# Optimization experiments

Measured on AMD Instinct MI355X. Metric: run time of the kernel, lower is better.

Reference implementation:

```python
import jax, jax.numpy as jnp
import numpy as np

B, N, C = 2, 2048, 1024
H = 16
HD = C // H  # 64


def setup_inputs() -> dict:
    key = jax.random.key(0)
    ks = jax.random.split(key, 6)
    x = jax.random.normal(ks[0], (B, N, C), dtype=jnp.float32)
    # realistic rotary angles
    inv_freq = 1.0 / (10000.0 ** (np.arange(0, HD, 2, dtype=np.float32) / HD))
    t = np.arange(N, dtype=np.float32)
    freqs = np.outer(t, inv_freq)                      # [N, HD/2]
    emb = np.concatenate([freqs, freqs], axis=-1)      # [N, HD]
    cos = jnp.asarray(np.cos(emb), dtype=jnp.float32)
    sin = jnp.asarray(np.sin(emb), dtype=jnp.float32)
    qkv_w = jax.random.normal(ks[1], (3 * C, C), dtype=jnp.float32) * (1.0 / np.sqrt(C))
    proj_w = jax.random.normal(ks[2], (C, C), dtype=jnp.float32) * (1.0 / np.sqrt(C))
    proj_b = jnp.zeros((C,), dtype=jnp.float32)
    return {"x": x, "cos": cos, "sin": sin, "qkv_w": qkv_w, "proj_w": proj_w, "proj_b": proj_b}


def _apply_rope(x, cos, sin):
    # x: [B, H, N, HD]; cos/sin: [N, HD] (broadcast over B, H)
    x1, x2 = jnp.split(x, 2, axis=-1)
    rotated = jnp.concatenate([-x2, x1], axis=-1)
    return x * cos + rotated * sin


def reference(x, cos, sin, qkv_w, proj_w, proj_b):
    b, n, c = x.shape
    scale = (c // H) ** (-0.5)
    qkv = jnp.einsum('bnc,dc->bnd', x, qkv_w)          # [B, N, 3C]
    qkv = qkv.reshape(b, n, 3, H, HD).transpose(2, 0, 3, 1, 4)  # [3, B, H, N, HD]
    q, k, v = qkv[0], qkv[1], qkv[2]
    q = _apply_rope(q, cos, sin)
    k = _apply_rope(k, cos, sin)
    attn = jnp.einsum('bhid,bhjd->bhij', q, k) * scale  # [B, H, N, N]
    attn = jax.nn.softmax(attn, axis=-1)
    out = jnp.einsum('bhij,bhjd->bhid', attn, v)        # [B, H, N, HD]
    out = out.transpose(0, 2, 1, 3).reshape(b, n, c)    # [B, N, C]
    return jnp.einsum('bnc,dc->bnd', out, proj_w) + proj_b
```

## Files before the change

### kernel.cpp

```cpp
#include <hip/hip_runtime.h>
#include <stdint.h>

typedef __bf16 bf16;
typedef bf16 bf16x8 __attribute__((ext_vector_type(8)));
typedef float f32x4 __attribute__((ext_vector_type(4)));
typedef float f32x16 __attribute__((ext_vector_type(16)));
typedef unsigned short u16x8 __attribute__((ext_vector_type(8)));
typedef unsigned short u16x4 __attribute__((ext_vector_type(4)));

__device__ __forceinline__ unsigned short f2bfu(float f) {
    union { bf16 h; unsigned short u; } x;
    x.h = (bf16)f;
    return x.u;
}
__device__ __forceinline__ float bfu2f(unsigned short u) {
    union { unsigned int i; float f; } x;
    x.i = ((unsigned int)u) << 16;
    return x.f;
}
__device__ __forceinline__ unsigned int pack2bf(float a, float b) {
    union { bf16 h[2]; unsigned int u; } x;
    x.h[0] = (bf16)a; x.h[1] = (bf16)b;
    return x.u;
}
__device__ __forceinline__ void pl32_swap(unsigned int &a, unsigned int &b) {
    asm volatile("v_permlane32_swap_b32 %0, %1" : "+v"(a), "+v"(b));
}

__device__ __forceinline__ void gld_lds16(const void* g, void* l) {
    __builtin_amdgcn_global_load_lds(
        (const __attribute__((address_space(1))) unsigned int*)(uintptr_t)g,
        (__attribute__((address_space(3))) unsigned int*)(unsigned int)(uintptr_t)l,
        16, 0, 0);
}

__global__ void cast_bf16_kernel(const float* __restrict__ in,
                                 unsigned short* __restrict__ out, int n8) {
    int i = blockIdx.x * blockDim.x + threadIdx.x;
    if (i >= n8) return;
    const f32x4* p = (const f32x4*)(in + (size_t)i * 8);
    f32x4 a = p[0], b = p[1];
    u16x8 o;
    o[0]=f2bfu(a[0]); o[1]=f2bfu(a[1]); o[2]=f2bfu(a[2]); o[3]=f2bfu(a[3]);
    o[4]=f2bfu(b[0]); o[5]=f2bfu(b[1]); o[6]=f2bfu(b[2]); o[7]=f2bfu(b[3]);
    *(u16x8*)(out + (size_t)i * 8) = o;
}

__global__ void rope_kernel(unsigned short* __restrict__ qkv,
                            const float* __restrict__ cosp,
                            const float* __restrict__ sinp) {
    int tid = blockIdx.x * blockDim.x + threadIdx.x;
    int i8  = tid & 3;
    int h   = (tid >> 2) & 15;
    int sel = (tid >> 6) & 1;
    int n   = (tid >> 7) & 2047;
    int b   = tid >> 18;
    size_t base = ((size_t)(b*2048 + n))*3072 + sel*1024 + h*64 + i8*8;
    u16x8 x1 = *(u16x8*)(qkv + base);
    u16x8 x2 = *(u16x8*)(qkv + base + 32);
    const f32x4* cp = (const f32x4*)(cosp + n*64 + i8*8);
    const f32x4* sp = (const f32x4*)(sinp + n*64 + i8*8);
    f32x4 c0 = cp[0], c1 = cp[1], s0 = sp[0], s1 = sp[1];
    float scale = sel ? 1.0f : (0.125f * 1.44269504088896f);
    u16x8 o1, o2;
#pragma unroll
    for (int j = 0; j < 8; j++) {
        float cc = (j < 4) ? c0[j] : c1[j-4];
        float ss = (j < 4) ? s0[j] : s1[j-4];
        float a = bfu2f(x1[j]), d = bfu2f(x2[j]);
        o1[j] = f2bfu((a*cc - d*ss) * scale);
        o2[j] = f2bfu((d*cc + a*ss) * scale);
    }
    *(u16x8*)(qkv + base)      = o1;
    *(u16x8*)(qkv + base + 32) = o2;
}

__global__ __launch_bounds__(512, 2) void gemm_qkv8(
    const unsigned short* __restrict__ A, const unsigned short* __restrict__ B,
    unsigned short* __restrict__ C, int M, int N, int K)
{
    extern __shared__ char smem[];
    int nwgx = gridDim.x;
    int nwg  = nwgx * gridDim.y;
    int orig = blockIdx.y * nwgx + blockIdx.x;
    int cpx  = nwg >> 3;
    int wg   = (orig & 7) * cpx + (orig >> 3);
    int bx = wg % nwgx, by = wg / nwgx;
    int m0 = by << 8, n0 = bx << 8;
    int t  = threadIdx.x;
    int wv = t >> 6, l = t & 63;
    int fr = l & 15, fq = l >> 4;
    int wm = (wv >> 2) << 7;
    int wn = (wv & 3) << 6;
    int aswz = (fr & 3) << 4;

    auto stage = [&](int kt, int bsel) {
        int k0 = kt << 5;
        char* base = smem + (bsel << 15);
#pragma unroll
        for (int j = 0; j < 2; ++j) {
            int y   = (j << 13) + t * 16;
            int ly  = y ^ (((y >> 6) & 3) << 4);
            int row = ly >> 6;
            int colu = (ly & 63) >> 1;
            gld_lds16(A + (size_t)(m0 + row) * K + k0 + colu,
                      base + ((j << 13) + (wv << 10)));
            gld_lds16(B + (size_t)(n0 + row) * K + k0 + colu,
                      base + 16384 + ((j << 13) + (wv << 10)));
        }
    };

    f32x4 acc[8][4];
#pragma unroll
    for (int m = 0; m < 8; ++m)
#pragma unroll
        for (int n = 0; n < 4; ++n) acc[m][n] = f32x4{0.f, 0.f, 0.f, 0.f};

    stage(0, 0);
    stage(1, 1);
    int cb = 0;
    for (int kt = 0; kt < 32; ++kt) {
        if (kt < 31) asm volatile("s_waitcnt vmcnt(4)" ::: "memory");
        else         asm volatile("s_waitcnt vmcnt(0)" ::: "memory");
        __builtin_amdgcn_s_barrier();
        if (kt + 2 < 32) {
            int sb = cb - 1; if (sb < 0) sb = 2;
            stage(kt + 2, sb);
        }
        const char* base = smem + (cb << 15);
        const char* Ab = base + ((wm + fr) << 6) + ((fq * 16) ^ aswz);
        const char* Bb = base + 16384 + ((wn + fr) << 6) + ((fq * 16) ^ aswz);
        bf16x8 bfr[4], af[4];
#pragma unroll
        for (int n = 0; n < 4; ++n) bfr[n] = *(const bf16x8*)(Bb + (n << 10));
#pragma unroll
        for (int m = 0; m < 4; ++m) af[m]  = *(const bf16x8*)(Ab + (m << 10));
        __builtin_amdgcn_s_barrier();
        __builtin_amdgcn_s_setprio(1);
#pragma unroll
        for (int m = 0; m < 4; ++m)
#pragma unroll
            for (int n = 0; n < 4; ++n)
                acc[m][n] = __builtin_amdgcn_mfma_f32_16x16x32_bf16(af[m], bfr[n], acc[m][n], 0, 0, 0);
        __builtin_amdgcn_s_setprio(0);
#pragma unroll
        for (int m = 0; m < 4; ++m) af[m] = *(const bf16x8*)(Ab + ((m + 4) << 10));
        __builtin_amdgcn_s_barrier();
        __builtin_amdgcn_s_setprio(1);
#pragma unroll
        for (int m = 0; m < 4; ++m)
#pragma unroll
            for (int n = 0; n < 4; ++n)
                acc[m + 4][n] = __builtin_amdgcn_mfma_f32_16x16x32_bf16(af[m], bfr[n], acc[m + 4][n], 0, 0, 0);
        __builtin_amdgcn_s_setprio(0);
        cb = (cb == 2) ? 0 : cb + 1;
    }
#pragma unroll
    for (int m = 0; m < 8; ++m)
#pragma unroll
        for (int n = 0; n < 4; ++n)
#pragma unroll
            for (int e = 0; e < 4; ++e) {
                int row = m0 + wm + m * 16 + fq * 4 + e;
                int col = n0 + wn + n * 16 + fr;
                C[(size_t)row * N + col] = f2bfu(acc[m][n][e]);
            }
}

template<int OUT_F32>
__global__ __launch_bounds__(256, 2) void gemm_bt(
    const unsigned short* __restrict__ A, const unsigned short* __restrict__ B,
    void* __restrict__ Cp, const float* __restrict__ bias,
    int M, int N, int K)
{
    __shared__ __align__(16) unsigned short As[2][128*32];
    __shared__ __align__(16) unsigned short Bs[2][128*32];
    int nwg  = gridDim.x * gridDim.y;
    int orig = blockIdx.y * gridDim.x + blockIdx.x;
    int qq = nwg >> 3, rr = nwg & 7;
    int xcd = orig & 7, idx = orig >> 3;
    int wg = (xcd < rr) ? (xcd*(qq+1) + idx) : (rr*(qq+1) + (xcd-rr)*qq + idx);
    int bx = wg % gridDim.x, by = wg / gridDim.x;
    int m0 = by * 128, n0 = bx * 128;
    int t = threadIdx.x;
    int w = t >> 6, l = t & 63;
    int c = l & 15, g = l >> 4;
    int wm = (w >> 1) * 64, wn = (w & 1) * 64;

    auto stage = [&](int kt, int bsel) {
#pragma unroll
        for (int r2 = 0; r2 < 2; ++r2) {
            int xb = w*2048 + r2*1024;
            int x  = xb + l*16;
            int row  = x >> 6;
            int colu = (x & 63) >> 1;
            int k0 = kt << 5;
            gld_lds16(A + (size_t)(m0+row)*K + k0 + colu, (void*)(As[bsel] + (xb >> 1)));
            gld_lds16(B + (size_t)(n0+row)*K + k0 + colu, (void*)(Bs[bsel] + (xb >> 1)));
        }
    };

    f32x4 acc[4][4];
#pragma unroll
    for (int i = 0; i < 4; i++)
#pragma unroll
        for (int j = 0; j < 4; j++) acc[i][j] = f32x4{0.f,0.f,0.f,0.f};

    int nkt = K >> 5;
    stage(0, 0);
    int cur = 0;
    for (int kt = 0; kt < nkt; ++kt) {
        __syncthreads();
        if (kt + 1 < nkt) stage(kt + 1, cur ^ 1);
        const unsigned short* Ab = As[cur] + wm*32;
        const unsigned short* Bb = Bs[cur] + wn*32;
        bf16x8 af[4], bfr[4];
#pragma unroll
        for (int i = 0; i < 4; i++) af[i]  = *(const bf16x8*)(Ab + (i*16+c)*32 + g*8);
#pragma unroll
        for (int i = 0; i < 4; i++) bfr[i] = *(const bf16x8*)(Bb + (i*16+c)*32 + g*8);
#pragma unroll
        for (int i = 0; i < 4; i++)
#pragma unroll
            for (int j = 0; j < 4; j++)
                acc[i][j] = __builtin_amdgcn_mfma_f32_16x16x32_bf16(af[i], bfr[j], acc[i][j], 0, 0, 0);
        cur ^= 1;
    }
#pragma unroll
    for (int i = 0; i < 4; i++)
#pragma unroll
        for (int j = 0; j < 4; j++)
#pragma unroll
            for (int e = 0; e < 4; e++) {
                int row = m0 + wm + i*16 + g*4 + e;
                int col = n0 + wn + j*16 + c;
                float v = acc[i][j][e];
                if (bias) v += bias[col];
                if (OUT_F32) ((float*)Cp)[(size_t)row*N + col] = v;
                else ((unsigned short*)Cp)[(size_t)row*N + col] = f2bfu(v);
            }
}

__global__ __launch_bounds__(256, 2) void attn_kernel(
    const unsigned short* __restrict__ qkv, unsigned short* __restrict__ outp)
{
    __shared__ __align__(16) unsigned short Ks[2][64*64];
    __shared__ __align__(16) unsigned short Vt[2][64*64];
    int bh = blockIdx.y;
    int b = bh >> 4, h = bh & 15;
    int q0 = blockIdx.x << 7;
    int t = threadIdx.x;
    int w = t >> 6, l = t & 63;
    int q = l & 31, hi = l >> 5;
    int qw = q0 + w*32;
    size_t bh_base = ((size_t)b*2048)*3072 + (size_t)h*64;

    auto stageK = [&](int kv0, int bsel) {
#pragma unroll
        for (int r2 = 0; r2 < 2; ++r2) {
            int xb = w*2048 + r2*1024;
            int x  = xb + l*16;
            int row  = x >> 7;
            int scolb = (x & 127) ^ ((row & 7) << 4);
            gld_lds16(qkv + bh_base + 1024 + (size_t)(kv0 + row)*3072 + (scolb >> 1),
                      (void*)(Ks[bsel] + (xb >> 1)));
        }
    };
    auto loadV = [&](int kv0, u16x8 &v0, u16x8 &v1) {
        int p  = t >> 3;
        int hb = (t & 7) << 3;
        const unsigned short* src = qkv + bh_base + 2048 + (size_t)(kv0 + 2*p)*3072 + hb;
        v0 = *(const u16x8*)src;
        v1 = *(const u16x8*)(src + 3072);
    };
    auto writeV = [&](const u16x8 &v0, const u16x8 &v1, int bsel) {
        int p  = t >> 3;
        int hb = (t & 7) << 3;
#pragma unroll
        for (int e = 0; e < 8; e++) {
            int hd = hb + e;
            int colb = (4*p) ^ ((((hd) ^ (hd >> 3)) & 7) << 4);
            *(unsigned int*)((char*)Vt[bsel] + hd*128 + colb) =
                (unsigned int)v0[e] | ((unsigned int)v1[e] << 16);
        }
    };

    bf16x8 qf[4];
#pragma unroll
    for (int dc = 0; dc < 4; dc++)
        qf[dc] = *(const bf16x8*)(qkv + bh_base + (size_t)(qw + q)*3072 + dc*16 + hi*8);

    f32x16 oacc[2];
#pragma unroll
    for (int e = 0; e < 16; e++) { oacc[0][e] = 0.f; oacc[1][e] = 0.f; }
    float lsum = 0.f;

    u16x8 vc0, vc1, vn0, vn1;
    stageK(0, 0);
    loadV(0, vc0, vc1);
    int cur = 0;

    for (int kvt = 0; kvt < 32; ++kvt) {
        writeV(vc0, vc1, cur);
        __syncthreads();
        if (kvt < 31) {
            int kv0n = (kvt + 1) << 6;
            stageK(kv0n, cur ^ 1);
            loadV(kv0n, vn0, vn1);
        }
        const char* ksb = (const char*)Ks[cur];
        const char* vtb = (const char*)Vt[cur];

#pragma unroll
        for (int sblk = 0; sblk < 2; ++sblk) {
            f32x16 st;
#pragma unroll
            for (int e = 0; e < 16; e++) st[e] = 0.f;
            int krow = sblk*32 + q;
            int ksw = (krow & 7) << 4;
#pragma unroll
            for (int dc = 0; dc < 4; ++dc) {
                bf16x8 kf = *(const bf16x8*)(ksb + krow*128 + ((dc*32 + hi*16) ^ ksw));
                st = __builtin_amdgcn_mfma_f32_32x32x16_bf16(kf, qf[dc], st, 0, 0, 0);
            }
            unsigned int wds[8];
#pragma unroll
            for (int m = 0; m < 8; m++) {
                float p0 = __builtin_amdgcn_exp2f(st[2*m]);
                float p1 = __builtin_amdgcn_exp2f(st[2*m+1]);
                lsum += p0 + p1;
                wds[m] = pack2bf(p0, p1);
            }
#pragma unroll
            for (int half = 0; half < 2; ++half) {
                unsigned int a0 = wds[half*4 + 0], b0 = wds[half*4 + 2];
                unsigned int a1 = wds[half*4 + 1], b1 = wds[half*4 + 3];
                pl32_swap(a0, b0);
                pl32_swap(a1, b1);
                union { unsigned int u[4]; bf16x8 v; } pf;
                pf.u[0] = a0; pf.u[1] = a1; pf.u[2] = b0; pf.u[3] = b1;
                int kc = sblk*2 + half;
#pragma unroll
                for (int hdblk = 0; hdblk < 2; ++hdblk) {
                    int hd = hdblk*32 + q;
                    int vsw = ((hd ^ (hd >> 3)) & 7) << 4;
                    bf16x8 vf = *(const bf16x8*)(vtb + hd*128 + ((kc*32 + hi*16) ^ vsw));
                    oacc[hdblk] = __builtin_amdgcn_mfma_f32_32x32x16_bf16(vf, pf.v, oacc[hdblk], 0, 0, 0);
                }
            }
        }
        vc0 = vn0; vc1 = vn1;
        cur ^= 1;
    }
    float ltot = lsum + __shfl_xor(lsum, 32, 64);
    float rinv = 1.0f / ltot;
    size_t orow = (size_t)(b*2048 + qw + q) * 1024 + h*64;
#pragma unroll
    for (int hdblk = 0; hdblk < 2; ++hdblk)
#pragma unroll
        for (int quad = 0; quad < 4; ++quad) {
            u16x4 o4;
#pragma unroll
            for (int j = 0; j < 4; j++)
                o4[j] = f2bfu(oacc[hdblk][quad*4 + j] * rinv);
            *(u16x4*)(outp + orow + hdblk*32 + quad*8 + hi*4) = o4;
        }
}

extern "C" void kernel_launch(void* const* d_in, const int* in_sizes, int n_in,
                              void* d_out, int out_size, void* d_ws, size_t ws_size,
                              hipStream_t stream) {
    const float* x      = (const float*)d_in[0];
    const float* cosp   = (const float*)d_in[1];
    const float* sinp   = (const float*)d_in[2];
    const float* qkv_w  = (const float*)d_in[3];
    const float* proj_w = (const float*)d_in[4];
    const float* proj_b = (const float*)d_in[5];

    char* ws = (char*)d_ws;
    unsigned short* xb     = (unsigned short*)(ws);
    unsigned short* wqkvb  = (unsigned short*)(ws + (size_t)(8u << 20));
    unsigned short* wprojb = (unsigned short*)(ws + (size_t)(14u << 20));
    unsigned short* qkvb   = (unsigned short*)(ws + (size_t)(16u << 20));
    unsigned short* attno  = xb;

    cast_bf16_kernel<<<2048, 256, 0, stream>>>(x, xb, 524288);
    cast_bf16_kernel<<<1536, 256, 0, stream>>>(qkv_w, wqkvb, 393216);
    cast_bf16_kernel<<<512, 256, 0, stream>>>(proj_w, wprojb, 131072);

    hipFuncSetAttribute((const void*)gemm_qkv8,
                        hipFuncAttributeMaxDynamicSharedMemorySize, 98304);
    gemm_qkv8<<<dim3(12, 16), 512, 98304, stream>>>(xb, wqkvb, qkvb, 4096, 3072, 1024);
    rope_kernel<<<2048, 256, 0, stream>>>(qkvb, cosp, sinp);
    attn_kernel<<<dim3(16, 32), 256, 0, stream>>>(qkvb, attno);
    gemm_bt<1><<<dim3(8, 32), 256, 0, stream>>>(attno, wprojb, d_out, proj_b, 4096, 1024, 1024);
}
```

Measured before the change: 135.2 us.

## Split KV range across two wave groups per attention block and merge via LDS

The attention block grows from 4 to 8 waves. Each group of 4 waves handles half of the KV tiles for the same 128 queries, with its own double-buffered K/V staging in a 64KB LDS array. Because the softmax uses no running max, the two partial outputs and row sums are merged by a plain add through LDS before normalisation and the store. This halves the serial KV loop per block and raises resident waves, at the cost of an extra LDS reduction and tighter register limits from launch_bounds(512,4), which may cause spills.

```diff
diff --git a/kernel.cpp b/kernel.cpp
--- a/kernel.cpp
+++ b/kernel.cpp
@@ -241,46 +241,51 @@
             }
 }
 
-__global__ __launch_bounds__(256, 2) void attn_kernel(
+__global__ __launch_bounds__(512, 4) void attn_kernel(
     const unsigned short* __restrict__ qkv, unsigned short* __restrict__ outp)
 {
-    __shared__ __align__(16) unsigned short Ks[2][64*64];
-    __shared__ __align__(16) unsigned short Vt[2][64*64];
+    __shared__ __align__(16) char lds[65536];
     int bh = blockIdx.y;
     int b = bh >> 4, h = bh & 15;
     int q0 = blockIdx.x << 7;
     int t = threadIdx.x;
     int w = t >> 6, l = t & 63;
+    int pair = w >> 2, wp = w & 3;
+    int tp = t & 255;
     int q = l & 31, hi = l >> 5;
-    int qw = q0 + w*32;
+    int qw = q0 + wp*32;
     size_t bh_base = ((size_t)b*2048)*3072 + (size_t)h*64;
 
+    auto kbase = [&](int bsel) -> char* { return lds + (((pair << 1) | bsel) << 13); };
+    auto vbase = [&](int bsel) -> char* { return lds + 32768 + (((pair << 1) | bsel) << 13); };
+
     auto stageK = [&](int kv0, int bsel) {
 #pragma unroll
         for (int r2 = 0; r2 < 2; ++r2) {
-            int xb = w*2048 + r2*1024;
+            int xb = wp*2048 + r2*1024;
             int x  = xb + l*16;
             int row  = x >> 7;
             int scolb = (x & 127) ^ ((row & 7) << 4);
             gld_lds16(qkv + bh_base + 1024 + (size_t)(kv0 + row)*3072 + (scolb >> 1),
-                      (void*)(Ks[bsel] + (xb >> 1)));
+                      kbase(bsel) + xb);
         }
     };
     auto loadV = [&](int kv0, u16x8 &v0, u16x8 &v1) {
-        int p  = t >> 3;
-        int hb = (t & 7) << 3;
+        int p  = tp >> 3;
+        int hb = (tp & 7) << 3;
         const unsigned short* src = qkv + bh_base + 2048 + (size_t)(kv0 + 2*p)*3072 + hb;
         v0 = *(const u16x8*)src;
         v1 = *(const u16x8*)(src + 3072);
     };
     auto writeV = [&](const u16x8 &v0, const u16x8 &v1, int bsel) {
-        int p  = t >> 3;
-        int hb = (t & 7) << 3;
+        int p  = tp >> 3;
+        int hb = (tp & 7) << 3;
+        char* vb = vbase(bsel);
 #pragma unroll
         for (int e = 0; e < 8; e++) {
             int hd = hb + e;
             int colb = (4*p) ^ ((((hd) ^ (hd >> 3)) & 7) << 4);
-            *(unsigned int*)((char*)Vt[bsel] + hd*128 + colb) =
+            *(unsigned int*)(vb + hd*128 + colb) =
                 (unsigned int)v0[e] | ((unsigned int)v1[e] << 16);
         }
     };
@@ -295,21 +300,22 @@
     for (int e = 0; e < 16; e++) { oacc[0][e] = 0.f; oacc[1][e] = 0.f; }
     float lsum = 0.f;
 
+    int tile0 = pair << 4;
     u16x8 vc0, vc1, vn0, vn1;
-    stageK(0, 0);
-    loadV(0, vc0, vc1);
+    stageK(tile0 << 6, 0);
+    loadV(tile0 << 6, vc0, vc1);
     int cur = 0;
 
-    for (int kvt = 0; kvt < 32; ++kvt) {
+    for (int it = 0; it < 16; ++it) {
         writeV(vc0, vc1, cur);
         __syncthreads();
-        if (kvt < 31) {
-            int kv0n = (kvt + 1) << 6;
+        if (it < 15) {
+            int kv0n = (tile0 + it + 1) << 6;
             stageK(kv0n, cur ^ 1);
             loadV(kv0n, vn0, vn1);
         }
-        const char* ksb = (const char*)Ks[cur];
-        const char* vtb = (const char*)Vt[cur];
+        const char* ksb = kbase(cur);
+        const char* vtb = vbase(cur);
 
 #pragma unroll
         for (int sblk = 0; sblk < 2; ++sblk) {
@@ -352,19 +358,44 @@
         vc0 = vn0; vc1 = vn1;
         cur ^= 1;
     }
-    float ltot = lsum + __shfl_xor(lsum, 32, 64);
-    float rinv = 1.0f / ltot;
-    size_t orow = (size_t)(b*2048 + qw + q) * 1024 + h*64;
-#pragma unroll
-    for (int hdblk = 0; hdblk < 2; ++hdblk)
-#pragma unroll
-        for (int quad = 0; quad < 4; ++quad) {
-            u16x4 o4;
-#pragma unroll
-            for (int j = 0; j < 4; j++)
-                o4[j] = f2bfu(oacc[hdblk][quad*4 + j] * rinv);
-            *(u16x4*)(outp + orow + hdblk*32 + quad*8 + hi*4) = o4;
-        }
+    float lt = lsum + __shfl_xor(lsum, 32, 64);
+
+    __syncthreads();
+    int cbase = ((wp << 6) + l) << 7;
+    int swl = (l & 7) << 4;
+    if (pair == 1) {
+#pragma unroll
+        for (int j = 0; j < 8; ++j) {
+            int hb = j >> 2, qd = j & 3;
+            f32x4 v = f32x4{oacc[hb][qd*4+0], oacc[hb][qd*4+1],
+                            oacc[hb][qd*4+2], oacc[hb][qd*4+3]};
+            *(f32x4*)(lds + cbase + ((j << 4) ^ swl)) = v;
+        }
+        ((float*)(lds + 32768))[(wp << 6) + l] = lt;
+    }
+    __syncthreads();
+    if (pair == 0) {
+#pragma unroll
+        for (int j = 0; j < 8; ++j) {
+            int hb = j >> 2, qd = j & 3;
+            f32x4 v = *(const f32x4*)(lds + cbase + ((j << 4) ^ swl));
+#pragma unroll
+            for (int e = 0; e < 4; ++e) oacc[hb][qd*4+e] += v[e];
+        }
+        lt += ((float*)(lds + 32768))[(wp << 6) + l];
+        float rinv = 1.0f / lt;
+        size_t orow = (size_t)(b*2048 + qw + q) * 1024 + h*64;
+#pragma unroll
+        for (int hdblk = 0; hdblk < 2; ++hdblk)
+#pragma unroll
+            for (int quad = 0; quad < 4; ++quad) {
+                u16x4 o4;
+#pragma unroll
+                for (int j = 0; j < 4; j++)
+                    o4[j] = f2bfu(oacc[hdblk][quad*4 + j] * rinv);
+                *(u16x4*)(outp + orow + hdblk*32 + quad*8 + hi*4) = o4;
+            }
+    }
 }
 
 extern "C" void kernel_launch(void* const* d_in, const int* in_sizes, int n_in,
@@ -392,6 +423,6 @@
                         hipFuncAttributeMaxDynamicSharedMemorySize, 98304);
     gemm_qkv8<<<dim3(12, 16), 512, 98304, stream>>>(xb, wqkvb, qkvb, 4096, 3072, 1024);
     rope_kernel<<<2048, 256, 0, stream>>>(qkvb, cosp, sinp);
-    attn_kernel<<<dim3(16, 32), 256, 0, stream>>>(qkvb, attno);
+    attn_kernel<<<dim3(16, 32), 512, 0, stream>>>(qkvb, attno);
     gemm_bt<1><<<dim3(8, 32), 256, 0, stream>>>(attno, wprojb, d_out, proj_b, 4096, 1024, 1024);
 }
```

New measurement: 132.6 us. About the same (-1.9%).
